# Performance work log

Hardware: AMD Instinct MI355X
Metric: run time of the kernel (lower is better)

## Reference

```python
import jax, jax.numpy as jnp
import numpy as np

B, N, M = 4, 8192, 8192

def setup_inputs() -> dict:
    key = jax.random.key(0)
    k1, k2 = jax.random.split(key)
    xyz1 = jax.random.normal(k1, (B, N, 3), dtype=jnp.float32)
    xyz2 = jax.random.normal(k2, (B, M, 3), dtype=jnp.float32)
    return {"xyz1": xyz1, "xyz2": xyz2}

def reference(xyz1, xyz2):
    # pairwise squared distances: (B, N, M)
    diff = xyz1[:, :, None, :] - xyz2[:, None, :, :]
    dist = jnp.sum(diff * diff, axis=-1)
    dist1 = jnp.min(dist, axis=2)  # (B, N) nearest in xyz2 for each point of xyz1
    dist2 = jnp.min(dist, axis=1)  # (B, M) nearest in xyz1 for each point of xyz2
    return jnp.mean(dist1) + jnp.mean(dist2)
```

## Files before the change

### kernel.cpp

```cpp
#include <hip/hip_runtime.h>

typedef __attribute__((ext_vector_type(8))) short short8;
typedef __attribute__((ext_vector_type(16))) float f32x16;

#define NB 8192
#define JT_REAL 256
#define JT_PAD  258
#define JC 8
#define ONE_BF 0x3F80
#define BIG_BF 0x7F7F

__device__ inline unsigned short bf_rne(float f) {
    unsigned u = __float_as_uint(f);
    return (unsigned short)((u + 0x7fffu + ((u >> 16) & 1u)) >> 16);
}
__device__ inline float bf_up(unsigned short h) { return __uint_as_float(((unsigned)h) << 16); }

__global__ __launch_bounds__(256) void pack_kernel(
    const float* __restrict__ xyz1, const float* __restrict__ xyz2,
    short8* __restrict__ bfrag, int* __restrict__ minws, float* __restrict__ out)
{
    int t = blockIdx.x * 256 + threadIdx.x;
    const int FRAGS = 8 * JT_PAD * 64;
    if (t < FRAGS) {
        int lane = t & 63;
        int jt   = (t >> 6) % JT_PAD;
        int sb   = t / (64 * JT_PAD);
        int set = sb >> 2, b = sb & 3;
        int n = lane & 31, half = lane >> 5;
        short8 v = {0, 0, 0, 0, 0, 0, 0, 0};
        if (jt >= JT_REAL) {
            if (half == 0) v[6] = (short)BIG_BF;
        } else {
            const float* src = (set == 0) ? xyz2 : xyz1;
            const float* q = src + ((size_t)b * NB + (size_t)jt * 32 + n) * 3;
            float x = q[0], y = q[1], z = q[2];
            float mx = -2.f * x, my = -2.f * y, mz = -2.f * z;
            float qsq = x * x + y * y + z * z;
            unsigned short mhx = bf_rne(mx), mhy = bf_rne(my), mhz = bf_rne(mz);
            if (half == 0) {
                unsigned short mlx = bf_rne(mx - bf_up(mhx));
                unsigned short mly = bf_rne(my - bf_up(mhy));
                unsigned short mlz = bf_rne(mz - bf_up(mhz));
                unsigned short qh  = bf_rne(qsq);
                unsigned short ql  = bf_rne(qsq - bf_up(qh));
                v[0] = (short)mhx; v[1] = (short)mlx;
                v[2] = (short)mhy; v[3] = (short)mly;
                v[4] = (short)mhz; v[5] = (short)mlz;
                v[6] = (short)qh;  v[7] = (short)ql;
            } else {
                v[0] = (short)mhx; v[1] = (short)mhy; v[2] = (short)mhz;
                v[3] = (short)ONE_BF; v[4] = (short)ONE_BF;
            }
        }
        bfrag[t] = v;
    }
    if (t < 2 * 4 * NB) minws[t] = 0x7F7F7F7F;
    if (t == 0) out[0] = 0.f;
}

__global__ __launch_bounds__(256, 4) void chamfer_mfma_kernel(
    const float* __restrict__ xyz1, const float* __restrict__ xyz2,
    const short8* __restrict__ bfrag, int* __restrict__ minws)
{
    const int z    = blockIdx.z;
    const int dir  = z >> 2;
    const int b    = z & 3;
    const int lane = threadIdx.x & 63;
    const int w    = threadIdx.x >> 6;
    const int half = lane >> 5;
    const int m    = lane & 31;

    const float* __restrict__ P = (dir == 0) ? xyz1 : xyz2;

    const int rowbase = blockIdx.x * 512 + w * 128;
    short8 a[4];
    #pragma unroll
    for (int t = 0; t < 4; ++t) {
        const float* p = P + ((size_t)b * NB + rowbase + t * 32 + m) * 3;
        float x = p[0], y = p[1], zc = p[2];
        float psq = x * x + y * y + zc * zc;
        unsigned short hx = bf_rne(x), hy = bf_rne(y), hz = bf_rne(zc);
        short8 v = {0, 0, 0, 0, 0, 0, 0, 0};
        if (half == 0) {
            v[0] = (short)hx; v[1] = (short)hx;
            v[2] = (short)hy; v[3] = (short)hy;
            v[4] = (short)hz; v[5] = (short)hz;
            v[6] = (short)ONE_BF; v[7] = (short)ONE_BF;
        } else {
            unsigned short lx = bf_rne(x - bf_up(hx));
            unsigned short ly = bf_rne(y - bf_up(hy));
            unsigned short lz = bf_rne(zc - bf_up(hz));
            unsigned short ph = bf_rne(psq);
            unsigned short pl = bf_rne(psq - bf_up(ph));
            v[0] = (short)lx; v[1] = (short)ly; v[2] = (short)lz;
            v[3] = (short)ph; v[4] = (short)pl;
        }
        a[t] = v;
    }

    float rmn[4][16];
    #pragma unroll
    for (int t = 0; t < 4; ++t)
        #pragma unroll
        for (int r = 0; r < 16; ++r) rmn[t][r] = 3.4e38f;

    const f32x16 zero16 = {0,0,0,0,0,0,0,0,0,0,0,0,0,0,0,0};

    const short8* __restrict__ bp = bfrag + (size_t)z * JT_PAD * 64;
    const int j0 = blockIdx.y * (JT_REAL / JC);

    short8 f0 = bp[(size_t)(j0 + 0) * 64 + lane];
    short8 f1 = bp[(size_t)(j0 + 1) * 64 + lane];
    for (int jt = j0; jt < j0 + JT_REAL / JC; jt += 2) {
        short8 g0 = bp[(size_t)(jt + 2) * 64 + lane];
        short8 g1 = bp[(size_t)(jt + 3) * 64 + lane];
        #pragma unroll
        for (int t = 0; t < 4; ++t) {
            f32x16 d0 = __builtin_amdgcn_mfma_f32_32x32x16_bf16(a[t], f0, zero16, 0, 0, 0);
            f32x16 d1 = __builtin_amdgcn_mfma_f32_32x32x16_bf16(a[t], f1, zero16, 0, 0, 0);
            #pragma unroll
            for (int r = 0; r < 16; ++r)
                rmn[t][r] = fminf(rmn[t][r], fminf(d0[r], d1[r]));
        }
        f0 = g0; f1 = g1;
    }

    #pragma unroll
    for (int t = 0; t < 4; ++t)
        #pragma unroll
        for (int r = 0; r < 16; ++r) {
            float v = rmn[t][r];
            #pragma unroll
            for (int off = 16; off > 0; off >>= 1)
                v = fminf(v, __shfl_xor(v, off, 32));
            rmn[t][r] = v;
        }

    int* __restrict__ base = minws + (dir == 0 ? (size_t)b * NB
                                               : (size_t)4 * NB + (size_t)b * NB);
    if (m == 0) {
        #pragma unroll
        for (int t = 0; t < 4; ++t)
            #pragma unroll
            for (int r = 0; r < 16; ++r) {
                int row = rowbase + t * 32 + 4 * half + (r & 3) + 8 * (r >> 2);
                atomicMin(base + row, __float_as_int(rmn[t][r]));
            }
    }
}

__global__ __launch_bounds__(256) void reduce_kernel(
    const int* __restrict__ minws, float* __restrict__ out,
    int BN, int total, float scale1, float scale2)
{
    int t = blockIdx.x * 256 + threadIdx.x;
    float v = 0.f;
    if (t < total)
        v = __int_as_float(minws[t]) * (t < BN ? scale1 : scale2);

    #pragma unroll
    for (int off = 32; off > 0; off >>= 1)
        v += __shfl_down(v, off, 64);

    __shared__ float ssum[4];
    const int lane = threadIdx.x & 63;
    const int wave = threadIdx.x >> 6;
    if (lane == 0) ssum[wave] = v;
    __syncthreads();

    if (threadIdx.x == 0) {
        float s = 0.f;
        #pragma unroll
        for (int wv = 0; wv < 4; ++wv) s += ssum[wv];
        atomicAdd(out, s);
    }
}

extern "C" void kernel_launch(void* const* d_in, const int* in_sizes, int n_in,
                              void* d_out, int out_size, void* d_ws, size_t ws_size,
                              hipStream_t stream) {
    const float* xyz1 = (const float*)d_in[0];
    const float* xyz2 = (const float*)d_in[1];
    float* out = (float*)d_out;

    const int B = 4;
    const int BN = B * NB, BM = B * NB;
    const int total = BN + BM;

    short8* bfrag = (short8*)d_ws;
    int* minws = (int*)(bfrag + (size_t)8 * JT_PAD * 64);

    const int FRAGS = 8 * JT_PAD * 64;
    pack_kernel<<<(FRAGS + 255) / 256, 256, 0, stream>>>(xyz1, xyz2, bfrag, minws, out);

    dim3 grid(16, JC, 2 * B);
    chamfer_mfma_kernel<<<grid, 256, 0, stream>>>(xyz1, xyz2, bfrag, minws);

    const float scale1 = 1.0f / (float)BN;
    const float scale2 = 1.0f / (float)BM;
    reduce_kernel<<<(total + 255) / 256, 256, 0, stream>>>(
        minws, out, BN, total, scale1, scale2);
}
```

Before: 99.58 us.

## Compute distance tiles once and reduce both row and column minima

Instead of launching both chamfer directions separately, each MFMA distance tile is now reduced along rows (kept in registers) and along columns (reduced in-register, then one cross-half shuffle and an atomicMin per column tile). This halves the MFMA work and the packed-fragment preparation. In exchange it adds per-iteration column reductions and global atomics, lowers the occupancy hint, and halves the grid size.

```diff
diff --git a/kernel.cpp b/kernel.cpp
--- a/kernel.cpp
+++ b/kernel.cpp
@@ -17,23 +17,21 @@
 __device__ inline float bf_up(unsigned short h) { return __uint_as_float(((unsigned)h) << 16); }
 
 __global__ __launch_bounds__(256) void pack_kernel(
-    const float* __restrict__ xyz1, const float* __restrict__ xyz2,
+    const float* __restrict__ xyz2,
     short8* __restrict__ bfrag, int* __restrict__ minws, float* __restrict__ out)
 {
     int t = blockIdx.x * 256 + threadIdx.x;
-    const int FRAGS = 8 * JT_PAD * 64;
+    const int FRAGS = 4 * JT_PAD * 64;
     if (t < FRAGS) {
         int lane = t & 63;
         int jt   = (t >> 6) % JT_PAD;
-        int sb   = t / (64 * JT_PAD);
-        int set = sb >> 2, b = sb & 3;
+        int b    = t / (64 * JT_PAD);
         int n = lane & 31, half = lane >> 5;
         short8 v = {0, 0, 0, 0, 0, 0, 0, 0};
         if (jt >= JT_REAL) {
             if (half == 0) v[6] = (short)BIG_BF;
         } else {
-            const float* src = (set == 0) ? xyz2 : xyz1;
-            const float* q = src + ((size_t)b * NB + (size_t)jt * 32 + n) * 3;
+            const float* q = xyz2 + ((size_t)b * NB + (size_t)jt * 32 + n) * 3;
             float x = q[0], y = q[1], z = q[2];
             float mx = -2.f * x, my = -2.f * y, mz = -2.f * z;
             float qsq = x * x + y * y + z * z;
@@ -59,25 +57,21 @@
     if (t == 0) out[0] = 0.f;
 }
 
-__global__ __launch_bounds__(256, 4) void chamfer_mfma_kernel(
-    const float* __restrict__ xyz1, const float* __restrict__ xyz2,
-    const short8* __restrict__ bfrag, int* __restrict__ minws)
+__global__ __launch_bounds__(256, 2) void chamfer_mfma_kernel(
+    const float* __restrict__ xyz1, const short8* __restrict__ bfrag,
+    int* __restrict__ minws)
 {
-    const int z    = blockIdx.z;
-    const int dir  = z >> 2;
-    const int b    = z & 3;
+    const int b    = blockIdx.z;
     const int lane = threadIdx.x & 63;
     const int w    = threadIdx.x >> 6;
     const int half = lane >> 5;
     const int m    = lane & 31;
 
-    const float* __restrict__ P = (dir == 0) ? xyz1 : xyz2;
-
     const int rowbase = blockIdx.x * 512 + w * 128;
     short8 a[4];
     #pragma unroll
     for (int t = 0; t < 4; ++t) {
-        const float* p = P + ((size_t)b * NB + rowbase + t * 32 + m) * 3;
+        const float* p = xyz1 + ((size_t)b * NB + rowbase + t * 32 + m) * 3;
         float x = p[0], y = p[1], zc = p[2];
         float psq = x * x + y * y + zc * zc;
         unsigned short hx = bf_rne(x), hy = bf_rne(y), hz = bf_rne(zc);
@@ -107,23 +101,41 @@
 
     const f32x16 zero16 = {0,0,0,0,0,0,0,0,0,0,0,0,0,0,0,0};
 
-    const short8* __restrict__ bp = bfrag + (size_t)z * JT_PAD * 64;
+    int* __restrict__ minrow = minws + (size_t)b * NB;
+    int* __restrict__ mincol = minws + (size_t)4 * NB + (size_t)b * NB;
+
+    const short8* __restrict__ bp = bfrag + (size_t)b * JT_PAD * 64;
     const int j0 = blockIdx.y * (JT_REAL / JC);
 
     short8 f0 = bp[(size_t)(j0 + 0) * 64 + lane];
     short8 f1 = bp[(size_t)(j0 + 1) * 64 + lane];
-    for (int jt = j0; jt < j0 + JT_REAL / JC; jt += 2) {
-        short8 g0 = bp[(size_t)(jt + 2) * 64 + lane];
-        short8 g1 = bp[(size_t)(jt + 3) * 64 + lane];
-        #pragma unroll
-        for (int t = 0; t < 4; ++t) {
-            f32x16 d0 = __builtin_amdgcn_mfma_f32_32x32x16_bf16(a[t], f0, zero16, 0, 0, 0);
-            f32x16 d1 = __builtin_amdgcn_mfma_f32_32x32x16_bf16(a[t], f1, zero16, 0, 0, 0);
+    for (int jt = j0; jt < j0 + JT_REAL / JC; ++jt) {
+        short8 g = bp[(size_t)(jt + 2) * 64 + lane];
+        f32x16 d[4];
+        #pragma unroll
+        for (int t = 0; t < 4; ++t)
+            d[t] = __builtin_amdgcn_mfma_f32_32x32x16_bf16(a[t], f0, zero16, 0, 0, 0);
+
+        #pragma unroll
+        for (int t = 0; t < 4; ++t)
             #pragma unroll
             for (int r = 0; r < 16; ++r)
-                rmn[t][r] = fminf(rmn[t][r], fminf(d0[r], d1[r]));
-        }
-        f0 = g0; f1 = g1;
+                rmn[t][r] = fminf(rmn[t][r], d[t][r]);
+
+        float cr[16];
+        #pragma unroll
+        for (int r = 0; r < 16; ++r)
+            cr[r] = fminf(fminf(d[0][r], d[1][r]), fminf(d[2][r], d[3][r]));
+        #pragma unroll
+        for (int s = 8; s > 0; s >>= 1)
+            #pragma unroll
+            for (int r = 0; r < s; ++r)
+                cr[r] = fminf(cr[r], cr[r + s]);
+        float cm = fminf(cr[0], __shfl_xor(cr[0], 32, 64));
+        if (half == 0)
+            atomicMin(mincol + jt * 32 + m, __float_as_int(cm));
+
+        f0 = f1; f1 = g;
     }
 
     #pragma unroll
@@ -137,15 +149,13 @@
             rmn[t][r] = v;
         }
 
-    int* __restrict__ base = minws + (dir == 0 ? (size_t)b * NB
-                                               : (size_t)4 * NB + (size_t)b * NB);
     if (m == 0) {
         #pragma unroll
         for (int t = 0; t < 4; ++t)
             #pragma unroll
             for (int r = 0; r < 16; ++r) {
                 int row = rowbase + t * 32 + 4 * half + (r & 3) + 8 * (r >> 2);
-                atomicMin(base + row, __float_as_int(rmn[t][r]));
+                atomicMin(minrow + row, __float_as_int(rmn[t][r]));
             }
     }
 }
@@ -189,13 +199,13 @@
     const int total = BN + BM;
 
     short8* bfrag = (short8*)d_ws;
-    int* minws = (int*)(bfrag + (size_t)8 * JT_PAD * 64);
-
-    const int FRAGS = 8 * JT_PAD * 64;
-    pack_kernel<<<(FRAGS + 255) / 256, 256, 0, stream>>>(xyz1, xyz2, bfrag, minws, out);
-
-    dim3 grid(16, JC, 2 * B);
-    chamfer_mfma_kernel<<<grid, 256, 0, stream>>>(xyz1, xyz2, bfrag, minws);
+    int* minws = (int*)(bfrag + (size_t)4 * JT_PAD * 64);
+
+    const int FRAGS = 4 * JT_PAD * 64;
+    pack_kernel<<<(FRAGS + 255) / 256, 256, 0, stream>>>(xyz2, bfrag, minws, out);
+
+    dim3 grid(16, JC, B);
+    chamfer_mfma_kernel<<<grid, 256, 0, stream>>>(xyz1, bfrag, minws);
 
     const float scale1 = 1.0f / (float)BN;
     const float scale2 = 1.0f / (float)BM;
```

Measured after the change: 106.2 us. 6.7% more time.
